# Kernel optimization log

Measured on AMD Instinct MI355X. Metric: run time of the kernel, lower is better.

The kernel has to match this reference:

```python
import jax, jax.numpy as jnp
import numpy as np

B, T, C, H = 8, 4096, 1024, 128  # batch, seq, n_embd, head_size


def setup_inputs() -> dict:
    key = jax.random.key(0)
    ks = jax.random.split(key, 4)
    std = 1.0 / np.sqrt(C)
    return {
        "x": jax.random.normal(ks[0], (B, T, C), dtype=jnp.float32),
        "Wq": jax.random.normal(ks[1], (C, H), dtype=jnp.float32) * std,
        "bq": jnp.zeros((H,), dtype=jnp.float32),
        "Wk": jax.random.normal(ks[2], (C, H), dtype=jnp.float32) * std,
        "bk": jnp.zeros((H,), dtype=jnp.float32),
        "Wv": jax.random.normal(ks[3], (C, H), dtype=jnp.float32) * std,
        "bv": jnp.zeros((H,), dtype=jnp.float32),
    }


def reference(x, Wq, bq, Wk, bk, Wv, bv):
    # Q, K, V projections: [B, T, H]
    q = x @ Wq + bq
    k = x @ Wk + bk
    v = x @ Wv + bv
    scale = jnp.asarray(H, x.dtype) ** -0.5
    # scaled attention scores: [B, T, T]
    wei = jnp.einsum("bqh,bkh->bqk", q, k) * scale
    # causal mask: position q attends to k <= q
    causal = jnp.tril(jnp.ones((T, T), dtype=bool))
    wei = jnp.where(causal[None, :, :], wei, jnp.finfo(x.dtype).min)
    wei = jax.nn.softmax(wei, axis=-1)
    # dropout p=0.0 (eval) -> identity
    out = jnp.einsum("bqk,bkh->bqh", wei, v)  # [B, T, H]
    return out
```

## Files before the change

### kernel.cpp

```cpp
#include <hip/hip_runtime.h>
#include <hip/hip_bf16.h>

typedef __attribute__((ext_vector_type(8))) short short8;
typedef __attribute__((ext_vector_type(4))) short shortx4;
typedef __attribute__((ext_vector_type(4))) float floatx4;
typedef __attribute__((ext_vector_type(4))) unsigned int uintx4;

#define BB 8
#define TT 4096
#define CC 1024
#define HH 128
#define BT (BB * TT)
#define MBASE 16.0f

__device__ __forceinline__ unsigned short f2bf(float f) {
    unsigned int u = __float_as_uint(f);
    u += 0x7fffu + ((u >> 16) & 1u);
    return (unsigned short)(u >> 16);
}

__device__ __forceinline__ void async16(const unsigned short* g, unsigned short* l) {
    __builtin_amdgcn_global_load_lds(
        (const __attribute__((address_space(1))) unsigned int*)g,
        (__attribute__((address_space(3))) unsigned int*)l, 16, 0, 0);
}

__global__ void conv_w(const float* __restrict__ Wq, const float* __restrict__ Wk,
                       const float* __restrict__ Wv, unsigned short* __restrict__ Wt) {
    __shared__ float tile[32][33];
    const int w = blockIdx.z, nt = blockIdx.y, kt = blockIdx.x;
    const int tx = threadIdx.x, ty = threadIdx.y;
    const float* W = (w == 0) ? Wq : ((w == 1) ? Wk : Wv);
#pragma unroll
    for (int i = 0; i < 4; ++i)
        tile[ty + 8 * i][tx] = W[(kt * 32 + ty + 8 * i) * HH + nt * 32 + tx];
    __syncthreads();
#pragma unroll
    for (int i = 0; i < 4; ++i)
        Wt[w * (HH * CC) + (nt * 32 + ty + 8 * i) * CC + kt * 32 + tx] = f2bf(tile[tx][ty + 8 * i]);
}

__global__ __launch_bounds__(256, 2) void proj_gemm(
    const float* __restrict__ x, const unsigned short* __restrict__ Wt,
    const float* __restrict__ bq, const float* __restrict__ bk, const float* __restrict__ bv,
    unsigned short* __restrict__ Qb, unsigned short* __restrict__ Kb,
    unsigned short* __restrict__ Vt) {
    __shared__ unsigned short Bs[3][192 * 64];
    const int gid = blockIdx.x;
    const int c = gid & 7, j = gid >> 3;
    const int mb = c * 32 + (j >> 1);
    const int nb = j & 1;
    const int tid = threadIdx.x, lane = tid & 63, wv = tid >> 6;
    const int quad = lane >> 4, l15 = lane & 15;
    const int brow = lane >> 3;
    const int wc = (lane & 7) ^ (brow & 7);
    const unsigned short* Wp = Wt + (long)nb * 192 * CC;
    const float* xw = x + ((long)mb * 128 + wv * 32 + l15) * CC + quad * 8;
    const int rw = mb * 128 + wv * 32;

    floatx4 acc[2][12];
#pragma unroll
    for (int i = 0; i < 2; ++i)
#pragma unroll
        for (int jj = 0; jj < 12; ++jj) {
            floatx4 z = {0.f, 0.f, 0.f, 0.f};
            acc[i][jj] = z;
        }

    floatx4 pf[8];
    short8 af[2][2];

    auto loadA = [&](int kt) {
#pragma unroll
        for (int mi = 0; mi < 2; ++mi)
#pragma unroll
            for (int ks = 0; ks < 2; ++ks) {
                const float* p = xw + (long)mi * 16 * CC + kt * 64 + ks * 32;
                pf[mi * 4 + ks * 2]     = *(const floatx4*)p;
                pf[mi * 4 + ks * 2 + 1] = *(const floatx4*)(p + 4);
            }
    };
    auto cvtA = [&]() {
#pragma unroll
        for (int mi = 0; mi < 2; ++mi)
#pragma unroll
            for (int ks = 0; ks < 2; ++ks) {
                floatx4 a = pf[mi * 4 + ks * 2], b2 = pf[mi * 4 + ks * 2 + 1];
                short8 r;
                r[0] = (short)f2bf(a[0]);  r[1] = (short)f2bf(a[1]);
                r[2] = (short)f2bf(a[2]);  r[3] = (short)f2bf(a[3]);
                r[4] = (short)f2bf(b2[0]); r[5] = (short)f2bf(b2[1]);
                r[6] = (short)f2bf(b2[2]); r[7] = (short)f2bf(b2[3]);
                af[mi][ks] = r;
            }
    };
    auto stageB = [&](int kt, int buf) {
#pragma unroll
        for (int h = 0; h < 6; ++h) {
            int grp = wv + 4 * h;
            async16(Wp + (long)(grp * 8 + brow) * CC + kt * 64 + wc * 8, &Bs[buf][grp * 512]);
        }
    };

    loadA(0);
    stageB(0, 0);
    stageB(1, 1);
    __builtin_amdgcn_sched_barrier(0);
    asm volatile("s_waitcnt vmcnt(6)" ::: "memory");
    __builtin_amdgcn_s_barrier();
    __builtin_amdgcn_sched_barrier(0);
    int cur = 0;

    for (int kt = 0; kt < 16; ++kt) {
        cvtA();
        if (kt < 15) loadA(kt + 1);
        __builtin_amdgcn_sched_barrier(0);
        if (kt < 14) {
            int b2 = cur ? cur - 1 : 2;
            stageB(kt + 2, b2);
        }
        __builtin_amdgcn_sched_barrier(0);

        const unsigned short* Bc = Bs[cur];
#pragma unroll
        for (int ks = 0; ks < 2; ++ks)
#pragma unroll
            for (int ni = 0; ni < 12; ++ni) {
                short8 bfr = *(const short8*)&Bc[(ni * 16 + l15) * 64 +
                                                 (((ks * 4 + quad) ^ (l15 & 7)) * 8)];
                acc[0][ni] = __builtin_amdgcn_mfma_f32_16x16x32_bf16(af[0][ks], bfr, acc[0][ni], 0, 0, 0);
                acc[1][ni] = __builtin_amdgcn_mfma_f32_16x16x32_bf16(af[1][ks], bfr, acc[1][ni], 0, 0, 0);
            }
        __builtin_amdgcn_sched_barrier(0);

        if (kt < 15) {
            if (kt < 14) { asm volatile("s_waitcnt vmcnt(14)" ::: "memory"); }
            else         { asm volatile("s_waitcnt vmcnt(8)"  ::: "memory"); }
            __builtin_amdgcn_s_barrier();
            __builtin_amdgcn_sched_barrier(0);
            cur = (cur == 2) ? 0 : cur + 1;
        }
    }

    const float qscale = 0.08838834764831845f * 1.4426950408889634f;
    unsigned short* Tw = &Bs[1][wv * 640];
#pragma unroll
    for (int ni = 0; ni < 12; ++ni) {
        int f = 12 * nb + ni;
        int col = f * 16 + l15;
        int h = col & 127;
        if (f < 16) {
            float bval = (f < 8) ? bq[h] : bk[h];
            unsigned short* dst = (f < 8) ? Qb : Kb;
#pragma unroll
            for (int mi = 0; mi < 2; ++mi)
#pragma unroll
                for (int r = 0; r < 4; ++r) {
                    int row = rw + mi * 16 + quad * 4 + r;
                    float v = acc[mi][ni][r] + bval;
                    if (f < 8) v *= qscale;
                    dst[(long)row * HH + h] = f2bf(v);
                }
        } else {
            float bval = bv[h];
#pragma unroll
            for (int mi = 0; mi < 2; ++mi) {
                shortx4 pk;
#pragma unroll
                for (int r = 0; r < 4; ++r) pk[r] = (short)f2bf(acc[mi][ni][r] + bval);
                *(shortx4*)&Tw[l15 * 40 + mi * 16 + quad * 4] = pk;
            }
            int th = lane >> 2, seg = lane & 3;
            uintx4 q0 = *(const uintx4*)&Tw[th * 40 + seg * 8];
            int hg = (f - 16) * 16 + th;
            int bb = rw >> 12, t0 = (rw & 4095) + seg * 8;
            unsigned short* vp = Vt + (long)bb * (HH * TT) + (long)hg * TT + t0;
            *(uintx4*)vp = q0;
        }
    }
}

__global__ __launch_bounds__(512, 2) void attn(
    const unsigned short* __restrict__ Qb, const unsigned short* __restrict__ Kb,
    const unsigned short* __restrict__ Vt, unsigned short* __restrict__ Op,
    float* __restrict__ Lh) {
    __shared__ unsigned short Ks[64 * 128];
    __shared__ unsigned short Vs[128 * 64];
    __shared__ unsigned short Ps[8 * 16 * 40];
    const int gid = blockIdx.x;
    const int b = gid & 7;
    const int idx = gid >> 3;
    const int qp = idx >> 2;
    const int s = idx & 3;
    const int qb0 = 62 - 2 * qp;
    const int len2 = qb0 + 2;
    const int lo = (s * len2) >> 2;
    const int hi = ((s + 1) * len2) >> 2;
    const int tid = threadIdx.x, lane = tid & 63, wv = tid >> 6;
    const int quad = lane >> 4, l15 = lane & 15;
    const int qb_w = qb0 + (wv >> 2);
    const int hi_eff = (hi < qb_w + 1) ? hi : qb_w + 1;

    short8 qf[4];
    {
        const unsigned short* qp_ = Qb + ((long)b * TT + qb0 * 64 + wv * 16 + l15) * HH + quad * 8;
#pragma unroll
        for (int ks = 0; ks < 4; ++ks) qf[ks] = *(const short8*)(qp_ + ks * 32);
    }
    floatx4 o[8];
#pragma unroll
    for (int i = 0; i < 8; ++i) {
        floatx4 z = {0.f, 0.f, 0.f, 0.f};
        o[i] = z;
    }
    float l_part[4] = {0.f, 0.f, 0.f, 0.f};

    const int kc = l15 ^ ((4 * wv + quad) & 15);
    const unsigned short* Kg = Kb + (long)b * TT * HH + ((long)lo * 64 + 4 * wv + quad) * HH + kc * 8;
    const int vrow = lane >> 3;
    const int vc = (lane & 7) ^ vrow;
    const unsigned short* Vg = Vt + (long)b * HH * TT + (long)(8 * wv + vrow) * TT + lo * 64 + vc * 8;
    unsigned short* Pw = &Ps[wv * 640];

    for (int kb = lo; kb < hi; ++kb) {
#pragma unroll
        for (int h = 0; h < 2; ++h) {
            int grp = 8 * h + wv;
            async16(Kg + (long)h * 32 * HH, &Ks[grp * 512]);
            async16(Vg + (long)h * 64 * TT, &Vs[grp * 512]);
        }
        Kg += (long)64 * HH;
        Vg += 64;
        __syncthreads();

        if (kb <= qb_w) {
            floatx4 sArr[4];
#pragma unroll
            for (int nt = 0; nt < 4; ++nt) {
                floatx4 z = {0.f, 0.f, 0.f, 0.f};
                sArr[nt] = z;
            }
            __builtin_amdgcn_s_setprio(1);
#pragma unroll
            for (int ks = 0; ks < 4; ++ks)
#pragma unroll
                for (int nt = 0; nt < 4; ++nt) {
                    short8 kf = *(const short8*)&Ks[(nt * 16 + l15) * 128 + (((ks * 4 + quad) ^ l15) * 8)];
                    sArr[nt] = __builtin_amdgcn_mfma_f32_16x16x32_bf16(qf[ks], kf, sArr[nt], 0, 0, 0);
                }
            __builtin_amdgcn_s_setprio(0);

            if (kb == qb_w) {
                int rowl = (wv & 3) * 16 + quad * 4;
#pragma unroll
                for (int nt = 0; nt < 4; ++nt) {
                    int col = nt * 16 + l15;
#pragma unroll
                    for (int r = 0; r < 4; ++r)
                        if (col > rowl + r) sArr[nt][r] = -1e30f;
                }
            }

#pragma unroll
            for (int nt = 0; nt < 4; ++nt)
#pragma unroll
                for (int r = 0; r < 4; ++r)
                    sArr[nt][r] = exp2f(sArr[nt][r] - MBASE);
#pragma unroll
            for (int r = 0; r < 4; ++r)
                l_part[r] += (sArr[0][r] + sArr[1][r]) + (sArr[2][r] + sArr[3][r]);

#pragma unroll
            for (int k2 = 0; k2 < 2; ++k2) {
#pragma unroll
                for (int ntl = 0; ntl < 2; ++ntl)
#pragma unroll
                    for (int r = 0; r < 4; ++r)
                        Pw[(quad * 4 + r) * 40 + ntl * 16 + l15] = f2bf(sArr[k2 * 2 + ntl][r]);
                short8 pfrag = *(const short8*)&Pw[l15 * 40 + quad * 8];
                __builtin_amdgcn_s_setprio(1);
#pragma unroll
                for (int hn = 0; hn < 8; ++hn) {
                    short8 vf = *(const short8*)&Vs[(hn * 16 + l15) * 64 +
                                                    (((k2 * 4 + quad) ^ (l15 & 7)) * 8)];
                    o[hn] = __builtin_amdgcn_mfma_f32_16x16x32_bf16(pfrag, vf, o[hn], 0, 0, 0);
                }
                __builtin_amdgcn_s_setprio(0);
            }
        }
        __syncthreads();
    }

    long rbase = (long)b * TT + qb0 * 64 + wv * 16 + quad * 4;
    unsigned short* Os = Op + (long)s * BT * HH;
    if (hi_eff > lo) {
#pragma unroll
        for (int hn = 0; hn < 8; ++hn)
#pragma unroll
            for (int r = 0; r < 4; ++r)
                Os[(rbase + r) * HH + hn * 16 + l15] = f2bf(o[hn][r]);
    }
#pragma unroll
    for (int r = 0; r < 4; ++r) {
        float l = l_part[r];
#pragma unroll
        for (int off = 1; off < 16; off <<= 1) l += __shfl_xor(l, off);
        if (l15 == 0) Lh[(long)s * BT + rbase + r] = (hi_eff > lo) ? l : 0.f;
    }
}

__global__ __launch_bounds__(256) void merge_kern(
    const unsigned short* __restrict__ Op, const float* __restrict__ Lh,
    float* __restrict__ out) {
    long e = ((long)blockIdx.x * 256 + threadIdx.x) * 8;
    long row = e >> 7;
    float lsum = Lh[row] + Lh[BT + row] + Lh[2 * (long)BT + row] + Lh[3 * (long)BT + row];
    float inv = 1.f / lsum;
    float acc[8];
#pragma unroll
    for (int j = 0; j < 8; ++j) acc[j] = 0.f;
#pragma unroll
    for (int s = 0; s < 4; ++s) {
        float ls = Lh[(long)s * BT + row];
        if (ls > 0.f) {
            uintx4 p = *(const uintx4*)(Op + (long)s * BT * HH + e);
#pragma unroll
            for (int j = 0; j < 4; ++j) {
                acc[2 * j]     += __uint_as_float(p[j] << 16);
                acc[2 * j + 1] += __uint_as_float(p[j] & 0xffff0000u);
            }
        }
    }
    floatx4 o0, o1;
#pragma unroll
    for (int j = 0; j < 4; ++j) {
        if (j < 2) { o0[2 * j] = acc[2 * j] * inv; o0[2 * j + 1] = acc[2 * j + 1] * inv; }
        else { o1[2 * (j - 2)] = acc[2 * j] * inv; o1[2 * (j - 2) + 1] = acc[2 * j + 1] * inv; }
    }
    *(floatx4*)(out + e) = o0;
    *(floatx4*)(out + e + 4) = o1;
}

extern "C" void kernel_launch(void* const* d_in, const int* in_sizes, int n_in,
                              void* d_out, int out_size, void* d_ws, size_t ws_size,
                              hipStream_t stream) {
    const float* x  = (const float*)d_in[0];
    const float* Wq = (const float*)d_in[1];
    const float* bq = (const float*)d_in[2];
    const float* Wk = (const float*)d_in[3];
    const float* bk = (const float*)d_in[4];
    const float* Wv = (const float*)d_in[5];
    const float* bv = (const float*)d_in[6];
    float* out = (float*)d_out;

    char* ws = (char*)d_ws;
    unsigned short* Wt = (unsigned short*)(ws);
    unsigned short* Qb = (unsigned short*)(ws + 1048576);
    unsigned short* Kb = (unsigned short*)(ws + 9437184);
    unsigned short* Vt = (unsigned short*)(ws + 17825792);
    unsigned short* Op = (unsigned short*)(ws + 26214400);
    float*          Lh = (float*)(ws + 59768832);

    conv_w<<<dim3(32, 4, 3), dim3(32, 8), 0, stream>>>(Wq, Wk, Wv, Wt);
    proj_gemm<<<512, 256, 0, stream>>>(x, Wt, bq, bk, bv, Qb, Kb, Vt);
    attn<<<1024, 512, 0, stream>>>(Qb, Kb, Vt, Op, Lh);
    merge_kern<<<2048, 256, 0, stream>>>(Op, Lh, out);
}
```

Measured before the change: 291.0 us.

## Double-buffer K/V tiles in attention and halve the split-K factor

The attention kernel now loads the next K/V tile into a second LDS buffer while the current one is being computed, replacing the load-then-sync loop with a prefetch pipeline. The key range is split two ways instead of four, so the grid halves and merge reads two partials. Blocks are ordered to pair long and short query tiles for balance, and launch bounds ask for higher occupancy. The trade-offs are double the LDS per block, fewer blocks to fill the GPU, and possible register pressure from the raised occupancy target.

```diff
diff --git a/kernel.cpp b/kernel.cpp
--- a/kernel.cpp
+++ b/kernel.cpp
@@ -180,22 +180,23 @@
     }
 }
 
-__global__ __launch_bounds__(512, 2) void attn(
+__global__ __launch_bounds__(512, 4) void attn(
     const unsigned short* __restrict__ Qb, const unsigned short* __restrict__ Kb,
     const unsigned short* __restrict__ Vt, unsigned short* __restrict__ Op,
     float* __restrict__ Lh) {
-    __shared__ unsigned short Ks[64 * 128];
-    __shared__ unsigned short Vs[128 * 64];
+    __shared__ unsigned short Ks[2][64 * 128];
+    __shared__ unsigned short Vs[2][128 * 64];
     __shared__ unsigned short Ps[8 * 16 * 40];
     const int gid = blockIdx.x;
     const int b = gid & 7;
     const int idx = gid >> 3;
-    const int qp = idx >> 2;
-    const int s = idx & 3;
+    const int s = idx & 1;
+    const int t = idx >> 1;
+    const int qp = (t < 16) ? t : 47 - t;
     const int qb0 = 62 - 2 * qp;
-    const int len2 = qb0 + 2;
-    const int lo = (s * len2) >> 2;
-    const int hi = ((s + 1) * len2) >> 2;
+    const int half = (qb0 + 2) >> 1;
+    const int lo = s * half;
+    const int hi = lo + half;
     const int tid = threadIdx.x, lane = tid & 63, wv = tid >> 6;
     const int quad = lane >> 4, l15 = lane & 15;
     const int qb_w = qb0 + (wv >> 2);
@@ -216,24 +217,36 @@
     float l_part[4] = {0.f, 0.f, 0.f, 0.f};
 
     const int kc = l15 ^ ((4 * wv + quad) & 15);
-    const unsigned short* Kg = Kb + (long)b * TT * HH + ((long)lo * 64 + 4 * wv + quad) * HH + kc * 8;
+    const unsigned short* Kg0 = Kb + (long)b * TT * HH + (long)(4 * wv + quad) * HH + kc * 8;
     const int vrow = lane >> 3;
     const int vc = (lane & 7) ^ vrow;
-    const unsigned short* Vg = Vt + (long)b * HH * TT + (long)(8 * wv + vrow) * TT + lo * 64 + vc * 8;
+    const unsigned short* Vg0 = Vt + (long)b * HH * TT + (long)(8 * wv + vrow) * TT + vc * 8;
     unsigned short* Pw = &Ps[wv * 640];
 
-    for (int kb = lo; kb < hi; ++kb) {
+    auto stage = [&](int kb2, int buf) {
 #pragma unroll
         for (int h = 0; h < 2; ++h) {
             int grp = 8 * h + wv;
-            async16(Kg + (long)h * 32 * HH, &Ks[grp * 512]);
-            async16(Vg + (long)h * 64 * TT, &Vs[grp * 512]);
-        }
-        Kg += (long)64 * HH;
-        Vg += 64;
-        __syncthreads();
+            async16(Kg0 + (long)kb2 * 64 * HH + (long)h * 32 * HH, &Ks[buf][grp * 512]);
+            async16(Vg0 + (long)kb2 * 64 + (long)h * 64 * TT, &Vs[buf][grp * 512]);
+        }
+    };
+
+    stage(lo, 0);
+    __builtin_amdgcn_sched_barrier(0);
+    asm volatile("s_waitcnt vmcnt(0)" ::: "memory");
+    __builtin_amdgcn_s_barrier();
+    __builtin_amdgcn_sched_barrier(0);
+    int cur = 0;
+
+    for (int kb = lo; kb < hi; ++kb) {
+        const bool pfetch = (kb + 1 < hi);
+        if (pfetch) stage(kb + 1, cur ^ 1);
+        __builtin_amdgcn_sched_barrier(0);
 
         if (kb <= qb_w) {
+            const unsigned short* Kc = Ks[cur];
+            const unsigned short* Vc = Vs[cur];
             floatx4 sArr[4];
 #pragma unroll
             for (int nt = 0; nt < 4; ++nt) {
@@ -245,7 +258,7 @@
             for (int ks = 0; ks < 4; ++ks)
 #pragma unroll
                 for (int nt = 0; nt < 4; ++nt) {
-                    short8 kf = *(const short8*)&Ks[(nt * 16 + l15) * 128 + (((ks * 4 + quad) ^ l15) * 8)];
+                    short8 kf = *(const short8*)&Kc[(nt * 16 + l15) * 128 + (((ks * 4 + quad) ^ l15) * 8)];
                     sArr[nt] = __builtin_amdgcn_mfma_f32_16x16x32_bf16(qf[ks], kf, sArr[nt], 0, 0, 0);
                 }
             __builtin_amdgcn_s_setprio(0);
@@ -281,14 +294,21 @@
                 __builtin_amdgcn_s_setprio(1);
 #pragma unroll
                 for (int hn = 0; hn < 8; ++hn) {
-                    short8 vf = *(const short8*)&Vs[(hn * 16 + l15) * 64 +
+                    short8 vf = *(const short8*)&Vc[(hn * 16 + l15) * 64 +
                                                     (((k2 * 4 + quad) ^ (l15 & 7)) * 8)];
                     o[hn] = __builtin_amdgcn_mfma_f32_16x16x32_bf16(pfrag, vf, o[hn], 0, 0, 0);
                 }
                 __builtin_amdgcn_s_setprio(0);
             }
         }
-        __syncthreads();
+
+        if (pfetch) {
+            __builtin_amdgcn_sched_barrier(0);
+            asm volatile("s_waitcnt vmcnt(0)" ::: "memory");
+            __builtin_amdgcn_s_barrier();
+            __builtin_amdgcn_sched_barrier(0);
+            cur ^= 1;
+        }
     }
 
     long rbase = (long)b * TT + qb0 * 64 + wv * 16 + quad * 4;
@@ -314,13 +334,13 @@
     float* __restrict__ out) {
     long e = ((long)blockIdx.x * 256 + threadIdx.x) * 8;
     long row = e >> 7;
-    float lsum = Lh[row] + Lh[BT + row] + Lh[2 * (long)BT + row] + Lh[3 * (long)BT + row];
+    float lsum = Lh[row] + Lh[BT + row];
     float inv = 1.f / lsum;
     float acc[8];
 #pragma unroll
     for (int j = 0; j < 8; ++j) acc[j] = 0.f;
 #pragma unroll
-    for (int s = 0; s < 4; ++s) {
+    for (int s = 0; s < 2; ++s) {
         float ls = Lh[(long)s * BT + row];
         if (ls > 0.f) {
             uintx4 p = *(const uintx4*)(Op + (long)s * BT * HH + e);
@@ -363,6 +383,6 @@
 
     conv_w<<<dim3(32, 4, 3), dim3(32, 8), 0, stream>>>(Wq, Wk, Wv, Wt);
     proj_gemm<<<512, 256, 0, stream>>>(x, Wt, bq, bk, bv, Qb, Kb, Vt);
-    attn<<<1024, 512, 0, stream>>>(Qb, Kb, Vt, Op, Lh);
+    attn<<<512, 512, 0, stream>>>(Qb, Kb, Vt, Op, Lh);
     merge_kern<<<2048, 256, 0, stream>>>(Op, Lh, out);
 }
```

Result: slower. 298.9 us (+2.7%).

## Split projection GEMM tile across eight waves of sixteen rows each

Applied to the files above, without the earlier changes.

The projection GEMM block grows from 256 to 512 threads, and each wave now computes a 16-row slice instead of 32 rows. That halves the per-wave accumulators and prefetch registers and spreads the B-tile staging over more waves. The intent is more resident waves per CU to hide global-load latency. In exchange each B fragment read from LDS now feeds one MFMA instead of two, so LDS traffic per FLOP doubles. The V transpose epilogue uses only half the lanes.

```diff
diff --git a/kernel.cpp b/kernel.cpp
--- a/kernel.cpp
+++ b/kernel.cpp
@@ -40,7 +40,7 @@
         Wt[w * (HH * CC) + (nt * 32 + ty + 8 * i) * CC + kt * 32 + tx] = f2bf(tile[tx][ty + 8 * i]);
 }
 
-__global__ __launch_bounds__(256, 2) void proj_gemm(
+__global__ __launch_bounds__(512, 4) void proj_gemm(
     const float* __restrict__ x, const unsigned short* __restrict__ Wt,
     const float* __restrict__ bq, const float* __restrict__ bk, const float* __restrict__ bv,
     unsigned short* __restrict__ Qb, unsigned short* __restrict__ Kb,
@@ -55,49 +55,43 @@
     const int brow = lane >> 3;
     const int wc = (lane & 7) ^ (brow & 7);
     const unsigned short* Wp = Wt + (long)nb * 192 * CC;
-    const float* xw = x + ((long)mb * 128 + wv * 32 + l15) * CC + quad * 8;
-    const int rw = mb * 128 + wv * 32;
-
-    floatx4 acc[2][12];
-#pragma unroll
-    for (int i = 0; i < 2; ++i)
-#pragma unroll
-        for (int jj = 0; jj < 12; ++jj) {
-            floatx4 z = {0.f, 0.f, 0.f, 0.f};
-            acc[i][jj] = z;
-        }
-
-    floatx4 pf[8];
-    short8 af[2][2];
+    const float* xw = x + ((long)mb * 128 + wv * 16 + l15) * CC + quad * 8;
+    const int rw = mb * 128 + wv * 16;
+
+    floatx4 acc[12];
+#pragma unroll
+    for (int jj = 0; jj < 12; ++jj) {
+        floatx4 z = {0.f, 0.f, 0.f, 0.f};
+        acc[jj] = z;
+    }
+
+    floatx4 pf[4];
+    short8 af[2];
 
     auto loadA = [&](int kt) {
 #pragma unroll
-        for (int mi = 0; mi < 2; ++mi)
-#pragma unroll
-            for (int ks = 0; ks < 2; ++ks) {
-                const float* p = xw + (long)mi * 16 * CC + kt * 64 + ks * 32;
-                pf[mi * 4 + ks * 2]     = *(const floatx4*)p;
-                pf[mi * 4 + ks * 2 + 1] = *(const floatx4*)(p + 4);
-            }
+        for (int ks = 0; ks < 2; ++ks) {
+            const float* p = xw + kt * 64 + ks * 32;
+            pf[ks * 2]     = *(const floatx4*)p;
+            pf[ks * 2 + 1] = *(const floatx4*)(p + 4);
+        }
     };
     auto cvtA = [&]() {
 #pragma unroll
-        for (int mi = 0; mi < 2; ++mi)
-#pragma unroll
-            for (int ks = 0; ks < 2; ++ks) {
-                floatx4 a = pf[mi * 4 + ks * 2], b2 = pf[mi * 4 + ks * 2 + 1];
-                short8 r;
-                r[0] = (short)f2bf(a[0]);  r[1] = (short)f2bf(a[1]);
-                r[2] = (short)f2bf(a[2]);  r[3] = (short)f2bf(a[3]);
-                r[4] = (short)f2bf(b2[0]); r[5] = (short)f2bf(b2[1]);
-                r[6] = (short)f2bf(b2[2]); r[7] = (short)f2bf(b2[3]);
-                af[mi][ks] = r;
-            }
+        for (int ks = 0; ks < 2; ++ks) {
+            floatx4 a = pf[ks * 2], b2 = pf[ks * 2 + 1];
+            short8 r;
+            r[0] = (short)f2bf(a[0]);  r[1] = (short)f2bf(a[1]);
+            r[2] = (short)f2bf(a[2]);  r[3] = (short)f2bf(a[3]);
+            r[4] = (short)f2bf(b2[0]); r[5] = (short)f2bf(b2[1]);
+            r[6] = (short)f2bf(b2[2]); r[7] = (short)f2bf(b2[3]);
+            af[ks] = r;
+        }
     };
     auto stageB = [&](int kt, int buf) {
 #pragma unroll
-        for (int h = 0; h < 6; ++h) {
-            int grp = wv + 4 * h;
+        for (int h = 0; h < 3; ++h) {
+            int grp = 8 * h + wv;
             async16(Wp + (long)(grp * 8 + brow) * CC + kt * 64 + wc * 8, &Bs[buf][grp * 512]);
         }
     };
@@ -106,7 +100,7 @@
     stageB(0, 0);
     stageB(1, 1);
     __builtin_amdgcn_sched_barrier(0);
-    asm volatile("s_waitcnt vmcnt(6)" ::: "memory");
+    asm volatile("s_waitcnt vmcnt(3)" ::: "memory");
     __builtin_amdgcn_s_barrier();
     __builtin_amdgcn_sched_barrier(0);
     int cur = 0;
@@ -128,14 +122,13 @@
             for (int ni = 0; ni < 12; ++ni) {
                 short8 bfr = *(const short8*)&Bc[(ni * 16 + l15) * 64 +
                                                  (((ks * 4 + quad) ^ (l15 & 7)) * 8)];
-                acc[0][ni] = __builtin_amdgcn_mfma_f32_16x16x32_bf16(af[0][ks], bfr, acc[0][ni], 0, 0, 0);
-                acc[1][ni] = __builtin_amdgcn_mfma_f32_16x16x32_bf16(af[1][ks], bfr, acc[1][ni], 0, 0, 0);
+                acc[ni] = __builtin_amdgcn_mfma_f32_16x16x32_bf16(af[ks], bfr, acc[ni], 0, 0, 0);
             }
         __builtin_amdgcn_sched_barrier(0);
 
         if (kt < 15) {
-            if (kt < 14) { asm volatile("s_waitcnt vmcnt(14)" ::: "memory"); }
-            else         { asm volatile("s_waitcnt vmcnt(8)"  ::: "memory"); }
+            if (kt < 14) { asm volatile("s_waitcnt vmcnt(7)" ::: "memory"); }
+            else         { asm volatile("s_waitcnt vmcnt(4)" ::: "memory"); }
             __builtin_amdgcn_s_barrier();
             __builtin_amdgcn_sched_barrier(0);
             cur = (cur == 2) ? 0 : cur + 1;
@@ -143,7 +136,7 @@
     }
 
     const float qscale = 0.08838834764831845f * 1.4426950408889634f;
-    unsigned short* Tw = &Bs[1][wv * 640];
+    unsigned short* Tw = &Bs[1][wv * 768];
 #pragma unroll
     for (int ni = 0; ni < 12; ++ni) {
         int f = 12 * nb + ni;
@@ -153,29 +146,26 @@
             float bval = (f < 8) ? bq[h] : bk[h];
             unsigned short* dst = (f < 8) ? Qb : Kb;
 #pragma unroll
-            for (int mi = 0; mi < 2; ++mi)
-#pragma unroll
-                for (int r = 0; r < 4; ++r) {
-                    int row = rw + mi * 16 + quad * 4 + r;
-                    float v = acc[mi][ni][r] + bval;
-                    if (f < 8) v *= qscale;
-                    dst[(long)row * HH + h] = f2bf(v);
-                }
+            for (int r = 0; r < 4; ++r) {
+                int row = rw + quad * 4 + r;
+                float v = acc[ni][r] + bval;
+                if (f < 8) v *= qscale;
+                dst[(long)row * HH + h] = f2bf(v);
+            }
         } else {
             float bval = bv[h];
-#pragma unroll
-            for (int mi = 0; mi < 2; ++mi) {
-                shortx4 pk;
-#pragma unroll
-                for (int r = 0; r < 4; ++r) pk[r] = (short)f2bf(acc[mi][ni][r] + bval);
-                *(shortx4*)&Tw[l15 * 40 + mi * 16 + quad * 4] = pk;
-            }
-            int th = lane >> 2, seg = lane & 3;
-            uintx4 q0 = *(const uintx4*)&Tw[th * 40 + seg * 8];
-            int hg = (f - 16) * 16 + th;
-            int bb = rw >> 12, t0 = (rw & 4095) + seg * 8;
-            unsigned short* vp = Vt + (long)bb * (HH * TT) + (long)hg * TT + t0;
-            *(uintx4*)vp = q0;
+            shortx4 pk;
+#pragma unroll
+            for (int r = 0; r < 4; ++r) pk[r] = (short)f2bf(acc[ni][r] + bval);
+            *(shortx4*)&Tw[l15 * 48 + quad * 4] = pk;
+            if (lane < 32) {
+                int th = lane >> 1, seg = lane & 1;
+                uintx4 q0 = *(const uintx4*)&Tw[th * 48 + seg * 8];
+                int hg = (f - 16) * 16 + th;
+                int bb = rw >> 12, t0 = (rw & 4095) + seg * 8;
+                unsigned short* vp = Vt + (long)bb * (HH * TT) + (long)hg * TT + t0;
+                *(uintx4*)vp = q0;
+            }
         }
     }
 }
@@ -362,7 +352,7 @@
     float*          Lh = (float*)(ws + 59768832);
 
     conv_w<<<dim3(32, 4, 3), dim3(32, 8), 0, stream>>>(Wq, Wk, Wv, Wt);
-    proj_gemm<<<512, 256, 0, stream>>>(x, Wt, bq, bk, bv, Qb, Kb, Vt);
+    proj_gemm<<<512, 512, 0, stream>>>(x, Wt, bq, bk, bv, Qb, Kb, Vt);
     attn<<<1024, 512, 0, stream>>>(Qb, Kb, Vt, Op, Lh);
     merge_kern<<<2048, 256, 0, stream>>>(Op, Lh, out);
 }
```

Result: no change. 290.6 us (-0.2%).
